# Performance work log

Hardware: AMD Instinct MI355X
Metric: run time of the kernel (lower is better)

Reference implementation:

```python
import jax, jax.numpy as jnp
import numpy as np

N, D, BS, M, DC, H, DH, L, E = 16384, 512, 16, 256, 512, 8, 64, 4, 262144
EPS = 1e-5


def _ln(x, w, b):
    mu = jnp.mean(x, -1, keepdims=True)
    var = jnp.var(x, -1, keepdims=True)
    return (x - mu) * jax.lax.rsqrt(var + EPS) * w + b


def _gcn(x, src, dst, W, b, n):
    deg = jax.ops.segment_sum(jnp.ones_like(src, dtype=x.dtype), dst, num_segments=n)
    dinv = jnp.where(deg > 0, deg ** -0.5, 0.0)
    norm = dinv[src] * dinv[dst]  # [E+N]
    h = x @ W
    out = jax.ops.segment_sum(h[src] * norm[:, None], dst, num_segments=n)
    return out + b


def _attn(xf, cond, Wq, Wk, Wv, Wo):
    n, d = xf.shape
    xb = xf.reshape(BS, n // BS, d)                    # stack(chunk(x, bs))
    q = (xb @ Wq).reshape(BS, -1, H, DH)
    k = (cond @ Wk).reshape(BS, -1, H, DH)
    v = (cond @ Wv).reshape(BS, -1, H, DH)
    att = jnp.einsum('bnhd,bmhd->bhnm', q, k) * (DH ** -0.5)
    w = jax.nn.softmax(att, axis=-1)
    o = jnp.einsum('bhnm,bmhd->bnhd', w, v).reshape(BS, -1, H * DH)
    return (o @ Wo).reshape(n, d)


def setup_inputs() -> dict:
    key = jax.random.key(0)
    ks = jax.random.split(key, 24)
    s = lambda fi, fo: (2.0 / (fi + fo)) ** 0.5
    inp = {
        'x': jax.random.normal(ks[0], (N, D), jnp.float32),
        'edge_index': jax.random.randint(ks[1], (2, E), 0, N, jnp.int64),
        'cond': jax.random.normal(ks[2], (BS, M, DC), jnp.float32),
        'bn_w': jnp.ones((D,), jnp.float32),
        'bn_b': jnp.zeros((D,), jnp.float32),
        'gcn_in_w': jax.random.normal(ks[3], (D, D), jnp.float32) * s(D, D),
        'gcn_in_b': jnp.zeros((D,), jnp.float32),
        'gcn_out_w': jax.random.normal(ks[4], (D, D), jnp.float32) * s(D, D),
        'gcn_out_b': jnp.zeros((D,), jnp.float32),
        'Wq': jax.random.normal(ks[5], (L, D, H * DH), jnp.float32) * s(D, H * DH),
        'Wk': jax.random.normal(ks[6], (L, DC, H * DH), jnp.float32) * s(DC, H * DH),
        'Wv': jax.random.normal(ks[7], (L, DC, H * DH), jnp.float32) * s(DC, H * DH),
        'Wo': jax.random.normal(ks[8], (L, H * DH, D), jnp.float32) * s(H * DH, D),
        'ln2_w': jnp.ones((L, D), jnp.float32),
        'ln2_b': jnp.zeros((L, D), jnp.float32),
        'ln3_w': jnp.ones((L, D), jnp.float32),
        'ln3_b': jnp.zeros((L, D), jnp.float32),
        'geglu_w': jax.random.normal(ks[9], (L, D, 8 * D), jnp.float32) * s(D, 8 * D),
        'geglu_b': jnp.zeros((L, 8 * D), jnp.float32),
        'ffo_w': jax.random.normal(ks[10], (L, 4 * D, D), jnp.float32) * s(4 * D, D),
        'ffo_b': jnp.zeros((L, D), jnp.float32),
    }
    return inp


def reference(x, edge_index, cond, bn_w, bn_b, gcn_in_w, gcn_in_b, gcn_out_w,
              gcn_out_b, Wq, Wk, Wv, Wo, ln2_w, ln2_b, ln3_w, ln3_b,
              geglu_w, geglu_b, ffo_w, ffo_b):
    n = x.shape[0]
    loops = jnp.arange(n)
    src = jnp.concatenate([edge_index[0], loops])
    dst = jnp.concatenate([edge_index[1], loops])

    x_in = x
    # BatchNorm1d (training mode: batch stats, biased var)
    mu = jnp.mean(x, 0)
    var = jnp.var(x, 0)
    h = (x - mu) * jax.lax.rsqrt(var + EPS) * bn_w + bn_b

    h = _gcn(h, src, dst, gcn_in_w, gcn_in_b, n)

    for i in range(L):
        a = _attn(_ln(h, ln2_w[i], ln2_b[i]), cond, Wq[i], Wk[i], Wv[i], Wo[i])
        h = h + a
        u = _ln(h, ln3_w[i], ln3_b[i]) @ geglu_w[i] + geglu_b[i]
        val, gate = jnp.split(u, 2, axis=-1)
        f = val * jax.nn.gelu(gate, approximate=False)
        h = h + f @ ffo_w[i] + ffo_b[i]

    h = _gcn(h, src, dst, gcn_out_w, gcn_out_b, n)
    return h + x_in
```

## Files before the change

kernel.cpp:

```cpp
#include <hip/hip_runtime.h>
#include <math.h>
#include <stdio.h>

#define N_NODES 16384
#define DIM     512
#define BSZ     16
#define SEQ     1024
#define MCTX    256
#define NHEAD   8
#define DHEAD   64
#define NLAYER  4
#define NEDGE   262144
#define DFF     2048
#define DG      4096
#define LNEPS   1e-5f

typedef unsigned short u16;
typedef __attribute__((ext_vector_type(8))) __bf16 bf16x8;
typedef __attribute__((ext_vector_type(4))) float f32x4;
typedef __attribute__((ext_vector_type(4))) unsigned short u16x4;
typedef __attribute__((ext_vector_type(8))) unsigned short u16x8;

__device__ __forceinline__ u16 f2b(float f) {
    unsigned u = __float_as_uint(f);
    unsigned r = (u + 0x7fff + ((u >> 16) & 1)) >> 16;
    return (u16)r;
}
__device__ __forceinline__ float b2f(u16 h) {
    return __uint_as_float((unsigned)h << 16);
}
__device__ __forceinline__ float gelu_exact(float x) {
    return 0.5f * x * (1.0f + erff(x * 0.70710678118654752f));
}
__device__ __forceinline__ float gelu_fast(float x) {
    float u = x * (0.7978845608f + 0.0356774081f * x * x);
    float e = __expf(2.f * u);
    float t = 1.f - 2.f / (e + 1.f);
    return 0.5f * x * (1.f + t);
}
__device__ __forceinline__ void gload16(const void* g, void* l) {
    __builtin_amdgcn_global_load_lds(
        (const __attribute__((address_space(1))) unsigned int*)g,
        (__attribute__((address_space(3))) unsigned int*)l, 16, 0, 0);
}

__device__ __forceinline__ int2 xcd_map() {
    int gx = gridDim.x, gy = gridDim.y;
    int nwg = gx * gy;
    int id = blockIdx.y * gx + blockIdx.x;
    int q = nwg >> 3, r = nwg & 7;
    int xcd = id & 7, idx = id >> 3;
    int nid = (xcd < r ? xcd * (q + 1) : r * (q + 1) + (xcd - r) * q) + idx;
    int2 o; o.x = nid % gx; o.y = nid / gx; return o;
}

__global__ __launch_bounds__(512, 2) void bgemm256_geglu(
    const u16* __restrict__ A, long lda,
    const u16* __restrict__ Bt, long ldb,
    const float* __restrict__ bias,
    u16* __restrict__ Cb, int K)
{
    __shared__ u16 lds[65536];

    const int t = threadIdx.x;
    const int w = t >> 6, lane = t & 63;
    const int fr = lane & 15, fq = lane >> 4;
    int2 sw = xcd_map();
    const int row0 = sw.y * 256;
    const int col0 = sw.x * 256;
    const int wm0 = (w >> 2) * 128, wn0 = (w & 3) * 64;
    const int sl = (lane & 7) ^ ((lane >> 3) & 7);

    f32x4 acc[8][4];
#pragma unroll
    for (int mf = 0; mf < 8; ++mf)
#pragma unroll
        for (int nf = 0; nf < 4; ++nf) acc[mf][nf] = (f32x4){0.f, 0.f, 0.f, 0.f};

    auto stageA = [&](int kt_, int P, int bb) {
        const int k0 = kt_ << 6;
#pragma unroll
        for (int rd = 0; rd < 2; ++rd) {
            int rbase = rd * 128 + P * 64 + w * 8;
            int r = rbase + (lane >> 3);
            gload16(A + (size_t)(row0 + r) * lda + k0 + sl * 8,
                    (char*)(lds + bb * 16384) + rbase * 128);
        }
    };
    auto stageB = [&](int kt_, int Q, int bb) {
        const int k0 = kt_ << 6;
#pragma unroll
        for (int rd = 0; rd < 2; ++rd) {
            int jb = rd * 64 + w * 8;
            int nbase = ((jb >> 5) << 6) + Q * 32 + (jb & 31);
            int n = nbase + (lane >> 3);
            gload16(Bt + (size_t)(col0 + n) * ldb + k0 + sl * 8,
                    (char*)(lds + 32768 + bb * 16384) + nbase * 128);
        }
    };

#define READ_A(MH, DST) do {                                                   \
    _Pragma("unroll")                                                          \
    for (int mi = 0; mi < 4; ++mi) {                                           \
        int r = wm0 + (MH) * 64 + mi * 16 + fr;                                \
        _Pragma("unroll")                                                      \
        for (int ks = 0; ks < 2; ++ks)                                         \
            DST[mi][ks] = *(const bf16x8*)&Ab_[r * 64 + (((ks*4+fq) ^ (fr&7)) * 8)]; \
    } } while (0)
#define READ_B(NH, DST) do {                                                   \
    _Pragma("unroll")                                                          \
    for (int ni = 0; ni < 2; ++ni) {                                           \
        int n = wn0 + (NH) * 32 + ni * 16 + fr;                                \
        _Pragma("unroll")                                                      \
        for (int ks = 0; ks < 2; ++ks)                                         \
            DST[ni][ks] = *(const bf16x8*)&Bb_[n * 64 + (((ks*4+fq) ^ (fr&7)) * 8)]; \
    } } while (0)
#define MFMA16(MH, NH, AV, BV)                                                 \
    _Pragma("unroll")                                                          \
    for (int mi = 0; mi < 4; ++mi)                                             \
        _Pragma("unroll")                                                      \
        for (int ni = 0; ni < 2; ++ni)                                         \
            _Pragma("unroll")                                                  \
            for (int ks = 0; ks < 2; ++ks)                                     \
                acc[(MH)*4+mi][(NH)*2+ni] = __builtin_amdgcn_mfma_f32_16x16x32_bf16( \
                    AV[mi][ks], BV[ni][ks], acc[(MH)*4+mi][(NH)*2+ni], 0, 0, 0)

    stageA(0, 0, 0); stageB(0, 0, 0); stageA(0, 1, 0); stageB(0, 1, 0);
    stageA(1, 0, 1); stageB(1, 0, 1);
    asm volatile("s_waitcnt vmcnt(4)" ::: "memory");
    __builtin_amdgcn_s_barrier();

    const int NT = K >> 6;
    for (int kt = 0; kt < NT; ++kt) {
        const int b = kt & 1;
        const bool s1 = (kt + 1 < NT), s2 = (kt + 2 < NT);
        const u16* Ab_ = lds + b * 16384;
        const u16* Bb_ = lds + 32768 + b * 16384;
        bf16x8 aR[4][2], bR[2][2], bK[2][2];

        READ_A(0, aR); READ_B(0, bK);
        if (s1) stageA(kt + 1, 1, b ^ 1);
        __builtin_amdgcn_s_barrier();
        asm volatile("s_waitcnt lgkmcnt(0)" ::: "memory");
        __builtin_amdgcn_s_setprio(1);
        MFMA16(0, 0, aR, bK);
        __builtin_amdgcn_s_setprio(0);
        __builtin_amdgcn_s_barrier();

        READ_B(1, bR);
        if (s1) stageB(kt + 1, 1, b ^ 1);
        __builtin_amdgcn_s_barrier();
        asm volatile("s_waitcnt lgkmcnt(0)" ::: "memory");
        __builtin_amdgcn_s_setprio(1);
        MFMA16(0, 1, aR, bR);
        __builtin_amdgcn_s_setprio(0);
        __builtin_amdgcn_s_barrier();

        READ_A(1, aR);
        if (s2) stageA(kt + 2, 0, b);
        __builtin_amdgcn_s_barrier();
        asm volatile("s_waitcnt lgkmcnt(0)" ::: "memory");
        __builtin_amdgcn_s_setprio(1);
        MFMA16(1, 1, aR, bR);
        __builtin_amdgcn_s_setprio(0);
        __builtin_amdgcn_s_barrier();

        if (s2) stageB(kt + 2, 0, b);
        __builtin_amdgcn_s_barrier();
        __builtin_amdgcn_s_setprio(1);
        MFMA16(1, 0, aR, bK);
        __builtin_amdgcn_s_setprio(0);
        if (s2)      asm volatile("s_waitcnt vmcnt(4)" ::: "memory");
        else if (s1) asm volatile("s_waitcnt vmcnt(0)" ::: "memory");
        __builtin_amdgcn_s_barrier();
    }
#undef READ_A
#undef READ_B
#undef MFMA16

    const int nbase = (col0 + wn0) >> 1;
    float bval[2], bgat[2];
#pragma unroll
    for (int P = 0; P < 2; ++P) {
        int n = nbase + P * 16 + fr;
        bval[P] = bias[n];
        bgat[P] = bias[DFF + n];
    }
#pragma unroll
    for (int mf = 0; mf < 8; ++mf) {
        const int rb = row0 + wm0 + mf * 16 + fq * 4;
#pragma unroll
        for (int P = 0; P < 2; ++P) {
            const int n = nbase + P * 16 + fr;
#pragma unroll
            for (int j = 0; j < 4; ++j) {
                float v = acc[mf][2 * P][j] + bval[P];
                float g = acc[mf][2 * P + 1][j] + bgat[P];
                Cb[(size_t)(rb + j) * DFF + n] = f2b(v * gelu_fast(g));
            }
        }
    }
}

template<int EPI>
__global__ __launch_bounds__(256) void bgemm(
    const u16* __restrict__ A, long lda,
    const u16* __restrict__ Bt, long ldb,
    const float* __restrict__ bias,
    const float* __restrict__ resid, long ldr,
    const float* __restrict__ rowscale,
    void* __restrict__ Cv, long ldc, int K, int nlo,
    long aHi, long aLo, long bHi, long bLo, long cHi, long cLo)
{
    __shared__ u16 lds[32768];

    const int t = threadIdx.x;
    const int z = blockIdx.z;
    const int zhi = z / nlo, zlo = z % nlo;
    const u16* Ag = A + (size_t)zhi * aHi + (size_t)zlo * aLo;
    const u16* Bg = Bt + (size_t)zhi * bHi + (size_t)zlo * bLo;
    const long coff = (long)zhi * cHi + (long)zlo * cLo;

    int2 sw = xcd_map();
    const int row0 = sw.y * 128;
    const int col0 = sw.x * 128;
    const int wave = t >> 6, lane = t & 63;
    const int wm0 = (wave >> 1) * 64, wn0 = (wave & 1) * 64;
    const int fr = lane & 15, fq = lane >> 4;
    const int ldsWave = (t & 192) * 16;
    const int rS = t >> 3;
    const int slotP = t & 7;

    f32x4 acc[4][4];
#pragma unroll
    for (int mi = 0; mi < 4; ++mi)
#pragma unroll
        for (int ni = 0; ni < 4; ++ni) acc[mi][ni] = (f32x4){0.f, 0.f, 0.f, 0.f};

    auto stage = [&](int buf, int k0) {
        u16* Ad = lds + buf * 8192;
        u16* Bd = lds + 16384 + buf * 8192;
#pragma unroll
        for (int i = 0; i < 4; ++i) {
            int r = i * 32 + rS;
            int s2 = slotP ^ (r & 7);
            gload16(Ag + (size_t)(row0 + r) * lda + k0 + s2 * 8,
                    (char*)Ad + i * 4096 + ldsWave);
        }
#pragma unroll
        for (int i = 0; i < 4; ++i) {
            int r = i * 32 + rS;
            int s2 = slotP ^ (r & 7);
            gload16(Bg + (size_t)(col0 + r) * ldb + k0 + s2 * 8,
                    (char*)Bd + i * 4096 + ldsWave);
        }
    };
    auto compute = [&](int buf) {
        const u16* Ac = lds + buf * 8192;
        const u16* Bc = lds + 16384 + buf * 8192;
#pragma unroll
        for (int ks = 0; ks < 2; ++ks) {
            const int ksl = ks * 4 + fq;
            bf16x8 av[4], bv[4];
#pragma unroll
            for (int mi = 0; mi < 4; ++mi) {
                int r = wm0 + mi * 16 + fr;
                av[mi] = *(const bf16x8*)&Ac[r * 64 + ((ksl ^ (r & 7)) * 8)];
            }
#pragma unroll
            for (int ni = 0; ni < 4; ++ni) {
                int r = wn0 + ni * 16 + fr;
                bv[ni] = *(const bf16x8*)&Bc[r * 64 + ((ksl ^ (r & 7)) * 8)];
            }
#pragma unroll
            for (int mi = 0; mi < 4; ++mi)
#pragma unroll
                for (int ni = 0; ni < 4; ++ni)
                    acc[mi][ni] = __builtin_amdgcn_mfma_f32_16x16x32_bf16(
                        av[mi], bv[ni], acc[mi][ni], 0, 0, 0);
        }
    };

    int cur = 0;
    stage(0, 0);
    __syncthreads();
    for (int k0 = 64; k0 < K; k0 += 64) {
        stage(cur ^ 1, k0);
        compute(cur);
        __syncthreads();
        cur ^= 1;
    }
    compute(cur);

    if (EPI == 3) {
        __syncthreads();
        u16* Tw = lds + wave * 4608;
#pragma unroll
        for (int mi = 0; mi < 4; ++mi)
#pragma unroll
            for (int ni = 0; ni < 4; ++ni)
#pragma unroll
                for (int j = 0; j < 4; ++j)
                    Tw[(ni * 16 + fr) * 72 + mi * 16 + fq * 4 + j] =
                        f2b(acc[mi][ni][j]);
        const int r0w = row0 + wm0;
        const int b = r0w >> 8, m0w = r0w & 255;
        const int cc0 = col0 + wn0, hh = cc0 >> 6;
        u16* dst = (u16*)Cv + coff + ((size_t)(b * 8 + hh) * 64) * 256 + m0w;
#pragma unroll
        for (int it = 0; it < 8; ++it) {
            int dl = it * 8 + (lane >> 3);
            int ml = (lane & 7) * 8;
            u16x8 v = *(const u16x8*)&Tw[dl * 72 + ml];
            *(u16x8*)&dst[(size_t)dl * 256 + ml] = v;
        }
        return;
    }

    float* Cf = (float*)Cv;
    u16* Cb = (u16*)Cv;
#pragma unroll
    for (int mi = 0; mi < 4; ++mi) {
        const int rb = row0 + wm0 + mi * 16 + fq * 4;
#pragma unroll
        for (int ni = 0; ni < 4; ++ni) {
            const int cc = col0 + wn0 + ni * 16 + fr;
            f32x4 v = acc[mi][ni];
            float bval = 0.f;
            if ((EPI == 1 || EPI == 2) && bias) bval = bias[cc];
#pragma unroll
            for (int j = 0; j < 4; ++j) {
                const long r = rb + j;
                float o = v[j] + bval;
                if (EPI == 1) {
                    Cb[coff + r * ldc + cc] = f2b(o);
                } else if (EPI == 2) {
                    Cf[coff + r * ldc + cc] = o + resid[r * ldr + cc];
                } else if (EPI == 4) {
                    Cb[coff + r * ldc + cc] = f2b(o * rowscale[r]);
                }
            }
        }
    }
}

__global__ __launch_bounds__(256) void transposeW(const float* __restrict__ src,
                                                  u16* __restrict__ dst,
                                                  int K, int N,
                                                  long srcZ, long dstZ, int permN)
{
    __shared__ float tile[64][65];
    const int t = threadIdx.x;
    const int n0 = blockIdx.x * 64, k0 = blockIdx.y * 64;
    const float* s = src + (size_t)blockIdx.z * srcZ;
    u16* d = dst + (size_t)blockIdx.z * dstZ;
#pragma unroll
    for (int i = 0; i < 16; ++i) {
        int idx = i * 256 + t;
        int rr = idx >> 6, cc = idx & 63;
        tile[rr][cc] = s[(size_t)(k0 + rr) * N + n0 + cc];
    }
    __syncthreads();
#pragma unroll
    for (int i = 0; i < 16; ++i) {
        int idx = i * 256 + t;
        int rr = idx >> 6, cc = idx & 63;
        int n = n0 + rr;
        int p = n;
        if (permN) {
            p = (n < permN) ? (((n >> 4) << 5) + (n & 15))
                            : ((((n - permN) >> 4) << 5) + 16 + ((n - permN) & 15));
        }
        d[(size_t)p * K + k0 + cc] = f2b(tile[cc][rr]);
    }
}

__global__ __launch_bounds__(256) void conv_f2b(const float* __restrict__ in,
                                                u16* __restrict__ out)
{
    size_t i = (size_t)blockIdx.x * 256 + threadIdx.x;
    float4 v = ((const float4*)in)[i];
    u16x4 o;
    o[0] = f2b(v.x); o[1] = f2b(v.y); o[2] = f2b(v.z); o[3] = f2b(v.w);
    ((u16x4*)out)[i] = o;
}

__global__ __launch_bounds__(512) void bn_colstats(const float* __restrict__ x,
                                                   float* __restrict__ cs,
                                                   float* __restrict__ cq)
{
    int c = threadIdx.x;
    int r0 = blockIdx.x * 128;
    float s = 0.f, q = 0.f;
    for (int r = 0; r < 128; ++r) {
        float v = x[(size_t)(r0 + r) * DIM + c];
        s += v; q += v * v;
    }
    atomicAdd(&cs[c], s);
    atomicAdd(&cq[c], q);
}

__global__ void bn_finalize(const float* __restrict__ cs, const float* __restrict__ cq,
                            const float* __restrict__ bw, const float* __restrict__ bb,
                            float* __restrict__ scale, float* __restrict__ shift)
{
    int c = threadIdx.x;
    float m   = cs[c] * (1.f / N_NODES);
    float var = cq[c] * (1.f / N_NODES) - m * m;
    float rs  = rsqrtf(var + LNEPS);
    float sc  = rs * bw[c];
    scale[c] = sc;
    shift[c] = bb[c] - m * sc;
}

__global__ __launch_bounds__(256) void bn_apply_b(const float* __restrict__ x,
                                                  const float* __restrict__ scale,
                                                  const float* __restrict__ shift,
                                                  u16* __restrict__ out)
{
    size_t idx = (size_t)blockIdx.x * 256 + threadIdx.x;
    int c4 = (int)(idx & 127);
    float4 v  = ((const float4*)x)[idx];
    float4 sc = ((const float4*)scale)[c4];
    float4 sh = ((const float4*)shift)[c4];
    u16x4 o;
    o[0] = f2b(v.x * sc.x + sh.x); o[1] = f2b(v.y * sc.y + sh.y);
    o[2] = f2b(v.z * sc.z + sh.z); o[3] = f2b(v.w * sc.w + sh.w);
    ((u16x4*)out)[idx] = o;
}

__global__ __launch_bounds__(256) void layernorm_b(const float* __restrict__ in,
                                                   const float* __restrict__ w,
                                                   const float* __restrict__ bsh,
                                                   u16* __restrict__ out)
{
    int lane = threadIdx.x & 63, wv = threadIdx.x >> 6;
    size_t row = (size_t)blockIdx.x * 4 + wv;
    const float* p = in + row * DIM + lane * 8;
    float4 v0 = *(const float4*)p;
    float4 v1 = *(const float4*)(p + 4);
    float s = v0.x + v0.y + v0.z + v0.w + v1.x + v1.y + v1.z + v1.w;
    float q = v0.x * v0.x + v0.y * v0.y + v0.z * v0.z + v0.w * v0.w +
              v1.x * v1.x + v1.y * v1.y + v1.z * v1.z + v1.w * v1.w;
    for (int m = 1; m < 64; m <<= 1) {
        s += __shfl_xor(s, m, 64);
        q += __shfl_xor(q, m, 64);
    }
    float mean = s * (1.f / DIM);
    float rs = rsqrtf(q * (1.f / DIM) - mean * mean + LNEPS);
    float4 w0 = *(const float4*)(w + lane * 8),   w1 = *(const float4*)(w + lane * 8 + 4);
    float4 b0 = *(const float4*)(bsh + lane * 8), b1 = *(const float4*)(bsh + lane * 8 + 4);
    u16x8 o;
    o[0] = f2b((v0.x - mean) * rs * w0.x + b0.x);
    o[1] = f2b((v0.y - mean) * rs * w0.y + b0.y);
    o[2] = f2b((v0.z - mean) * rs * w0.z + b0.z);
    o[3] = f2b((v0.w - mean) * rs * w0.w + b0.w);
    o[4] = f2b((v1.x - mean) * rs * w1.x + b1.x);
    o[5] = f2b((v1.y - mean) * rs * w1.y + b1.y);
    o[6] = f2b((v1.z - mean) * rs * w1.z + b1.z);
    o[7] = f2b((v1.w - mean) * rs * w1.w + b1.w);
    *(u16x8*)(out + row * DIM + lane * 8) = o;
}

__global__ __launch_bounds__(256) void fused_attn(
    const u16* __restrict__ Q,
    const u16* __restrict__ Kp,
    const u16* __restrict__ Vt,
    u16* __restrict__ O)
{
    __shared__ u16 Ks[256 * 64];
    __shared__ u16 Vs[64 * 256];
    __shared__ u16 Ps[4][16 * 256];

    const int t = threadIdx.x;
    const int wave = t >> 6, lane = t & 63;
    const int fr = lane & 15, fq = lane >> 4;
    const int qc = blockIdx.x, h = blockIdx.y, b = blockIdx.z;
    const int ldsW = (t & 192) * 16;

#pragma unroll
    for (int i = 0; i < 8; ++i) {
        int idx = i * 256 + t;
        int m = idx >> 3, s = idx & 7;
        gload16(Kp + (size_t)(b * MCTX + m) * 512 + h * 64 + ((s ^ (m & 7)) * 8),
                (char*)Ks + i * 4096 + ldsW);
    }
#pragma unroll
    for (int i = 0; i < 8; ++i) {
        int idx = i * 256 + t;
        int d = idx >> 5, s = idx & 31;
        gload16(Vt + (size_t)((b * 8 + h) * 64 + d) * 256 + ((s ^ (d & 7)) * 8),
                (char*)Vs + i * 4096 + ldsW);
    }
    __syncthreads();

    u16* Pw = Ps[wave];
    for (int it = 0; it < 4; ++it) {
        const int q0 = qc * 256 + it * 64 + wave * 16;
        bf16x8 aq[2];
#pragma unroll
        for (int ks = 0; ks < 2; ++ks)
            aq[ks] = *(const bf16x8*)&Q[(size_t)(b * SEQ + q0 + fr) * 512 +
                                        h * 64 + ks * 32 + fq * 8];
        f32x4 accS[16];
#pragma unroll
        for (int ni = 0; ni < 16; ++ni) accS[ni] = (f32x4){0.f, 0.f, 0.f, 0.f};
#pragma unroll
        for (int ni = 0; ni < 16; ++ni) {
            int m = ni * 16 + fr;
#pragma unroll
            for (int ks = 0; ks < 2; ++ks) {
                bf16x8 bv = *(const bf16x8*)&Ks[m * 64 + (((ks * 4 + fq) ^ (m & 7)) * 8)];
                accS[ni] = __builtin_amdgcn_mfma_f32_16x16x32_bf16(
                    aq[ks], bv, accS[ni], 0, 0, 0);
            }
        }
        const float cs = 0.125f;
#pragma unroll
        for (int j = 0; j < 4; ++j) {
            float m0 = accS[0][j];
#pragma unroll
            for (int ni = 1; ni < 16; ++ni) m0 = fmaxf(m0, accS[ni][j]);
            m0 = fmaxf(m0, __shfl_xor(m0, 1, 64));
            m0 = fmaxf(m0, __shfl_xor(m0, 2, 64));
            m0 = fmaxf(m0, __shfl_xor(m0, 4, 64));
            m0 = fmaxf(m0, __shfl_xor(m0, 8, 64));
            float s0 = 0.f;
#pragma unroll
            for (int ni = 0; ni < 16; ++ni) {
                float p = __expf((accS[ni][j] - m0) * cs);
                accS[ni][j] = p;
                s0 += p;
            }
            s0 += __shfl_xor(s0, 1, 64);
            s0 += __shfl_xor(s0, 2, 64);
            s0 += __shfl_xor(s0, 4, 64);
            s0 += __shfl_xor(s0, 8, 64);
            float inv = 1.f / s0;
#pragma unroll
            for (int ni = 0; ni < 16; ++ni) {
                int cc = ni * 16 + fr;
                int rr = fq * 4 + j;
                Pw[rr * 256 + (((cc >> 3) ^ (rr & 7)) * 8) + (cc & 7)] =
                    f2b(accS[ni][j] * inv);
            }
        }
        bf16x8 ap[8];
#pragma unroll
        for (int ks = 0; ks < 8; ++ks)
            ap[ks] = *(const bf16x8*)&Pw[fr * 256 + (((ks * 4 + fq) ^ (fr & 7)) * 8)];
        f32x4 accO[4];
#pragma unroll
        for (int ni = 0; ni < 4; ++ni) accO[ni] = (f32x4){0.f, 0.f, 0.f, 0.f};
#pragma unroll
        for (int ni = 0; ni < 4; ++ni) {
            int d = ni * 16 + fr;
#pragma unroll
            for (int ks = 0; ks < 8; ++ks) {
                bf16x8 bv = *(const bf16x8*)&Vs[d * 256 + (((ks * 4 + fq) ^ (d & 7)) * 8)];
                accO[ni] = __builtin_amdgcn_mfma_f32_16x16x32_bf16(
                    ap[ks], bv, accO[ni], 0, 0, 0);
            }
        }
#pragma unroll
        for (int ni = 0; ni < 4; ++ni)
#pragma unroll
            for (int j = 0; j < 4; ++j)
                O[(size_t)(b * SEQ + q0 + fq * 4 + j) * 512 + h * 64 + ni * 16 + fr] =
                    f2b(accO[ni][j]);
    }
}

__global__ void detect_i64(const int* __restrict__ e, int* __restrict__ flag)
{
    int idx = blockIdx.x * blockDim.x + threadIdx.x;
    if (e[2 * idx + 1] != 0) flag[0] = 1;
}

__global__ void deg_count(const int* __restrict__ eb, const int* __restrict__ flag,
                          int* __restrict__ deg)
{
    int e = blockIdx.x * blockDim.x + threadIdx.x;
    int d;
    if (flag[0]) d = eb[NEDGE + e];
    else         d = (int)((const long long*)eb)[NEDGE + e];
    atomicAdd(&deg[d], 1);
}

__global__ void dinv_k(const int* __restrict__ deg, float* __restrict__ dinv)
{
    int i = blockIdx.x * blockDim.x + threadIdx.x;
    dinv[i] = rsqrtf((float)(deg[i] + 1));
}

__global__ __launch_bounds__(1024) void scan_deg(const int* __restrict__ deg,
                                                 int* __restrict__ off)
{
    __shared__ int sums[1024];
    int t = threadIdx.x;
    int base = t * 16;
    int v[16]; int s = 0;
#pragma unroll
    for (int i = 0; i < 16; ++i) { v[i] = deg[base + i]; s += v[i]; }
    sums[t] = s;
    __syncthreads();
    for (int ofs = 1; ofs < 1024; ofs <<= 1) {
        int x = (t >= ofs) ? sums[t - ofs] : 0;
        __syncthreads();
        sums[t] += x;
        __syncthreads();
    }
    int run = (t == 0) ? 0 : sums[t - 1];
#pragma unroll
    for (int i = 0; i < 16; ++i) { off[base + i] = run; run += v[i]; }
    if (t == 1023) off[N_NODES] = run;
}

__global__ void fill_k(const int* __restrict__ eb, const int* __restrict__ flag,
                       const int* __restrict__ off, int* __restrict__ cursor,
                       int* __restrict__ csr)
{
    int e = blockIdx.x * blockDim.x + threadIdx.x;
    int s, d;
    if (flag[0]) { s = eb[e]; d = eb[NEDGE + e]; }
    else {
        const long long* p = (const long long*)eb;
        s = (int)p[e]; d = (int)p[NEDGE + e];
    }
    int pos = atomicAdd(&cursor[d], 1);
    csr[off[d] + pos] = s;
}

__global__ __launch_bounds__(256) void gcn_gather(
    const u16* __restrict__ h2, const int* __restrict__ csr,
    const int* __restrict__ off, const float* __restrict__ dinv,
    const float* __restrict__ bias, const float* __restrict__ addx,
    float* __restrict__ out)
{
    int lane = threadIdx.x & 63, wv = threadIdx.x >> 6;
    int d = blockIdx.x * 4 + wv;
    float acc[8];
#pragma unroll
    for (int j = 0; j < 8; ++j) acc[j] = 0.f;
    int e0 = off[d], e1 = off[d + 1];
    float dd = dinv[d];
    int sidx = (e0 < e1) ? csr[e0] : d;
    u16x8 v = *(const u16x8*)&h2[(size_t)sidx * DIM + lane * 8];
    for (int e = e0; e < e1; ++e) {
        int snext = (e + 1 < e1) ? csr[e + 1] : d;
        u16x8 vn = *(const u16x8*)&h2[(size_t)snext * DIM + lane * 8];
#pragma unroll
        for (int j = 0; j < 8; ++j) acc[j] += b2f(v[j]);
        v = vn;
    }
#pragma unroll
    for (int j = 0; j < 8; ++j) acc[j] = (acc[j] + b2f(v[j])) * dd;
    float o[8];
#pragma unroll
    for (int j = 0; j < 8; ++j) {
        o[j] = acc[j] + bias[lane * 8 + j];
        if (addx) o[j] += addx[(size_t)d * DIM + lane * 8 + j];
    }
    float* op = out + (size_t)d * DIM + lane * 8;
    *(float4*)op = make_float4(o[0], o[1], o[2], o[3]);
    *(float4*)(op + 4) = make_float4(o[4], o[5], o[6], o[7]);
}

extern "C" void kernel_launch(void* const* d_in, const int* in_sizes, int n_in,
                              void* d_out, int out_size, void* d_ws, size_t ws_size,
                              hipStream_t stream)
{
    const float* x         = (const float*)d_in[0];
    const int*   edges     = (const int*)d_in[1];
    const float* cond      = (const float*)d_in[2];
    const float* bn_w      = (const float*)d_in[3];
    const float* bn_b      = (const float*)d_in[4];
    const float* gcn_in_w  = (const float*)d_in[5];
    const float* gcn_in_b  = (const float*)d_in[6];
    const float* gcn_out_w = (const float*)d_in[7];
    const float* gcn_out_b = (const float*)d_in[8];
    const float* Wq  = (const float*)d_in[9];
    const float* Wk  = (const float*)d_in[10];
    const float* Wv  = (const float*)d_in[11];
    const float* Wo  = (const float*)d_in[12];
    const float* ln2w = (const float*)d_in[13];
    const float* ln2b = (const float*)d_in[14];
    const float* ln3w = (const float*)d_in[15];
    const float* ln3b = (const float*)d_in[16];
    const float* ggw = (const float*)d_in[17];
    const float* ggb = (const float*)d_in[18];
    const float* fow = (const float*)d_in[19];
    const float* fob = (const float*)d_in[20];
    float* outp = (float*)d_out;

    char* wsb = (char*)d_ws;
    size_t wsoff = 0;
    auto alloc = [&](size_t bytes) -> void* {
        void* p = wsb + wsoff;
        wsoff = (wsoff + bytes + 255) & ~(size_t)255;
        return p;
    };
    u16*   wT    = (u16*)  alloc((size_t)17301504 * 2);
    u16*   condb = (u16*)  alloc((size_t)4096 * 512 * 2);
    float* h     = (float*)alloc((size_t)N_NODES * DIM * 4);
    u16*   t0b   = (u16*)  alloc((size_t)N_NODES * DIM * 2);
    u16*   qb    = (u16*)  alloc((size_t)N_NODES * DIM * 2);
    u16*   ob    = (u16*)  alloc((size_t)N_NODES * DIM * 2);
    u16*   kb    = (u16*)  alloc((size_t)NLAYER * 4096 * 512 * 2);
    u16*   Vt    = (u16*)  alloc((size_t)NLAYER * BSZ * NHEAD * DHEAD * MCTX * 2);
    char*  zbase  = wsb + wsoff;
    float* colsum = (float*)alloc(DIM * 4);
    float* colsq  = (float*)alloc(DIM * 4);
    int*   deg    = (int*)  alloc(N_NODES * 4);
    int*   cursor = (int*)  alloc(N_NODES * 4);
    int*   eflag  = (int*)  alloc(256);
    size_t zbytes = (size_t)((wsb + wsoff) - zbase);
    float* bscale = (float*)alloc(DIM * 4);
    float* bshift = (float*)alloc(DIM * 4);
    float* dinv   = (float*)alloc(N_NODES * 4);
    int*   csr_off= (int*)  alloc((N_NODES + 16) * 4);
    int*   csr_src= (int*)  alloc((size_t)NEDGE * 4);

    int nch = 0;
    for (int c = 1; c <= 16; c *= 2) {
        size_t need = ((size_t)N_NODES / c) * DFF * 2;
        if (wsoff + need <= ws_size) { nch = c; break; }
    }
    if (nch == 0) { fprintf(stderr, "ws too small (%zu)\n", ws_size); return; }
    u16* Abuf = (u16*)(wsb + wsoff);

    hipMemsetAsync(zbase, 0, zbytes, stream);

    u16* gcnInT  = wT;
    u16* gcnOutT = gcnInT + 262144;
    u16* WqT = gcnOutT + 262144;
    u16* WkT = WqT + 4 * 262144;
    u16* WvT = WkT + 4 * 262144;
    u16* WoT = WvT + 4 * 262144;
    u16* ggT = WoT + 4 * 262144;
    u16* foT = ggT + 4 * 2097152;
    transposeW<<<dim3(8, 8, 1), 256, 0, stream>>>(gcn_in_w,  gcnInT, 512, 512, 0, 0, 0);
    transposeW<<<dim3(8, 8, 1), 256, 0, stream>>>(gcn_out_w, gcnOutT, 512, 512, 0, 0, 0);
    transposeW<<<dim3(8, 8, 4), 256, 0, stream>>>(Wq, WqT, 512, 512, 262144, 262144, 0);
    transposeW<<<dim3(8, 8, 4), 256, 0, stream>>>(Wk, WkT, 512, 512, 262144, 262144, 0);
    transposeW<<<dim3(8, 8, 4), 256, 0, stream>>>(Wv, WvT, 512, 512, 262144, 262144, 0);
    transposeW<<<dim3(8, 8, 4), 256, 0, stream>>>(Wo, WoT, 512, 512, 262144, 262144, 0);
    transposeW<<<dim3(64, 8, 4), 256, 0, stream>>>(ggw, ggT, 512, DG, 2097152, 2097152, DFF);
    transposeW<<<dim3(8, 32, 4), 256, 0, stream>>>(fow, foT, DFF, 512, 1048576, 1048576, 0);
    conv_f2b<<<2048, 256, 0, stream>>>(cond, condb);

    bn_colstats<<<128, 512, 0, stream>>>(x, colsum, colsq);
    bn_finalize<<<1, 512, 0, stream>>>(colsum, colsq, bn_w, bn_b, bscale, bshift);
    bn_apply_b<<<(N_NODES * DIM / 4) / 256, 256, 0, stream>>>(x, bscale, bshift, t0b);

    detect_i64<<<NEDGE / 256, 256, 0, stream>>>(edges, eflag);
    deg_count<<<NEDGE / 256, 256, 0, stream>>>(edges, eflag, deg);
    dinv_k<<<N_NODES / 256, 256, 0, stream>>>(deg, dinv);
    scan_deg<<<1, 1024, 0, stream>>>(deg, csr_off);
    fill_k<<<NEDGE / 256, 256, 0, stream>>>(edges, eflag, csr_off, cursor, csr_src);

    bgemm<1><<<dim3(4, 32, 4), 256, 0, stream>>>(
        condb, 512, WkT, 512, nullptr, nullptr, 0, nullptr, kb, 512, 512, 1,
        0, 0, 262144, 0, (long)4096 * 512, 0);
    bgemm<3><<<dim3(4, 32, 4), 256, 0, stream>>>(
        condb, 512, WvT, 512, nullptr, nullptr, 0, nullptr, Vt, 0, 512, 1,
        0, 0, 262144, 0, (long)BSZ * NHEAD * DHEAD * MCTX, 0);

    bgemm<4><<<dim3(4, 128, 1), 256, 0, stream>>>(
        t0b, 512, gcnInT, 512, nullptr, nullptr, 0, dinv, qb, 512, 512, 1,
        0, 0, 0, 0, 0, 0);
    gcn_gather<<<N_NODES / 4, 256, 0, stream>>>(qb, csr_src, csr_off, dinv,
                                                gcn_in_b, nullptr, h);

    const int ffrows = N_NODES / nch;
    for (int i = 0; i < NLAYER; ++i) {
        const u16* WqTi = WqT + (size_t)i * 262144;
        const u16* WoTi = WoT + (size_t)i * 262144;
        const u16* ggTi = ggT + (size_t)i * 2097152;
        const u16* foTi = foT + (size_t)i * 1048576;
        const u16* kbi  = kb + (size_t)i * 4096 * 512;
        const u16* Vti  = Vt + (size_t)i * BSZ * NHEAD * DHEAD * MCTX;

        layernorm_b<<<N_NODES / 4, 256, 0, stream>>>(h, ln2w + i * DIM, ln2b + i * DIM, t0b);
        bgemm<1><<<dim3(4, 128, 1), 256, 0, stream>>>(
            t0b, 512, WqTi, 512, nullptr, nullptr, 0, nullptr, qb, 512, 512, 1,
            0, 0, 0, 0, 0, 0);
        fused_attn<<<dim3(4, 8, 16), 256, 0, stream>>>(qb, kbi, Vti, ob);
        bgemm<2><<<dim3(4, 128, 1), 256, 0, stream>>>(
            ob, 512, WoTi, 512, nullptr, h, 512, nullptr, h, 512, 512, 1,
            0, 0, 0, 0, 0, 0);

        layernorm_b<<<N_NODES / 4, 256, 0, stream>>>(h, ln3w + i * DIM, ln3b + i * DIM, t0b);
        for (int c = 0; c < nch; ++c) {
            const u16* ac = t0b + (size_t)c * ffrows * 512;
            float* hc = h + (size_t)c * ffrows * 512;
            bgemm256_geglu<<<dim3(DG / 256, ffrows / 256), 512, 0, stream>>>(
                ac, 512, ggTi, 512, ggb + (size_t)i * DG, Abuf, 512);
            bgemm<2><<<dim3(4, ffrows / 128, 1), 256, 0, stream>>>(
                Abuf, 2048, foTi, 2048, fob + (size_t)i * DIM, hc, 512, nullptr,
                hc, 512, 2048, 1, 0, 0, 0, 0, 0, 0);
        }
    }

    conv_f2b<<<8192, 256, 0, stream>>>(h, t0b);
    bgemm<4><<<dim3(4, 128, 1), 256, 0, stream>>>(
        t0b, 512, gcnOutT, 512, nullptr, nullptr, 0, dinv, qb, 512, 512, 1,
        0, 0, 0, 0, 0, 0);
    gcn_gather<<<N_NODES / 4, 256, 0, stream>>>(qb, csr_src, csr_off, dinv,
                                                gcn_out_b, x, outp);
}
```

Before: 1.235 ms.

## Restructure GEGLU GEMM k-loop into two phases, stage epilogue via LDS, unroll GCN gather

The GEGLU GEMM main loop now reads all B fragments at once and runs two larger MFMA phases instead of four, issuing A and B staging loads together. This halves the barrier count per k-tile but raises register pressure. The GEGLU epilogue writes results to LDS and then stores coalesced 16-byte rows instead of scattered 2-byte stores. The GCN gather is unrolled by two with independent accumulators and loads the self-loop row separately, giving more memory-level parallelism.

```diff
diff --git a/kernel.cpp b/kernel.cpp
--- a/kernel.cpp
+++ b/kernel.cpp
@@ -107,23 +107,23 @@
         for (int ks = 0; ks < 2; ++ks)                                         \
             DST[mi][ks] = *(const bf16x8*)&Ab_[r * 64 + (((ks*4+fq) ^ (fr&7)) * 8)]; \
     } } while (0)
-#define READ_B(NH, DST) do {                                                   \
+#define READ_B_ALL(DST) do {                                                   \
     _Pragma("unroll")                                                          \
-    for (int ni = 0; ni < 2; ++ni) {                                           \
-        int n = wn0 + (NH) * 32 + ni * 16 + fr;                                \
+    for (int ni = 0; ni < 4; ++ni) {                                           \
+        int n = wn0 + ni * 16 + fr;                                            \
         _Pragma("unroll")                                                      \
         for (int ks = 0; ks < 2; ++ks)                                         \
             DST[ni][ks] = *(const bf16x8*)&Bb_[n * 64 + (((ks*4+fq) ^ (fr&7)) * 8)]; \
     } } while (0)
-#define MFMA16(MH, NH, AV, BV)                                                 \
+#define MFMA32(MH, AV, BV)                                                     \
     _Pragma("unroll")                                                          \
     for (int mi = 0; mi < 4; ++mi)                                             \
         _Pragma("unroll")                                                      \
-        for (int ni = 0; ni < 2; ++ni)                                         \
+        for (int ni = 0; ni < 4; ++ni)                                         \
             _Pragma("unroll")                                                  \
             for (int ks = 0; ks < 2; ++ks)                                     \
-                acc[(MH)*4+mi][(NH)*2+ni] = __builtin_amdgcn_mfma_f32_16x16x32_bf16( \
-                    AV[mi][ks], BV[ni][ks], acc[(MH)*4+mi][(NH)*2+ni], 0, 0, 0)
+                acc[(MH)*4+mi][ni] = __builtin_amdgcn_mfma_f32_16x16x32_bf16(  \
+                    AV[mi][ks], BV[ni][ks], acc[(MH)*4+mi][ni], 0, 0, 0)
 
     stageA(0, 0, 0); stageB(0, 0, 0); stageA(0, 1, 0); stageB(0, 1, 0);
     stageA(1, 0, 1); stageB(1, 0, 1);
@@ -136,47 +136,31 @@
         const bool s1 = (kt + 1 < NT), s2 = (kt + 2 < NT);
         const u16* Ab_ = lds + b * 16384;
         const u16* Bb_ = lds + 32768 + b * 16384;
-        bf16x8 aR[4][2], bR[2][2], bK[2][2];
-
-        READ_A(0, aR); READ_B(0, bK);
-        if (s1) stageA(kt + 1, 1, b ^ 1);
+        bf16x8 av[4][2], bv[4][2];
+
+        READ_A(0, av); READ_B_ALL(bv);
+        if (s1) { stageA(kt + 1, 1, b ^ 1); stageB(kt + 1, 1, b ^ 1); }
         __builtin_amdgcn_s_barrier();
         asm volatile("s_waitcnt lgkmcnt(0)" ::: "memory");
         __builtin_amdgcn_s_setprio(1);
-        MFMA16(0, 0, aR, bK);
+        MFMA32(0, av, bv);
         __builtin_amdgcn_s_setprio(0);
         __builtin_amdgcn_s_barrier();
 
-        READ_B(1, bR);
-        if (s1) stageB(kt + 1, 1, b ^ 1);
+        READ_A(1, av);
+        if (s2) { stageA(kt + 2, 0, b); stageB(kt + 2, 0, b); }
         __builtin_amdgcn_s_barrier();
         asm volatile("s_waitcnt lgkmcnt(0)" ::: "memory");
         __builtin_amdgcn_s_setprio(1);
-        MFMA16(0, 1, aR, bR);
-        __builtin_amdgcn_s_setprio(0);
-        __builtin_amdgcn_s_barrier();
-
-        READ_A(1, aR);
-        if (s2) stageA(kt + 2, 0, b);
-        __builtin_amdgcn_s_barrier();
-        asm volatile("s_waitcnt lgkmcnt(0)" ::: "memory");
-        __builtin_amdgcn_s_setprio(1);
-        MFMA16(1, 1, aR, bR);
-        __builtin_amdgcn_s_setprio(0);
-        __builtin_amdgcn_s_barrier();
-
-        if (s2) stageB(kt + 2, 0, b);
-        __builtin_amdgcn_s_barrier();
-        __builtin_amdgcn_s_setprio(1);
-        MFMA16(1, 0, aR, bK);
+        MFMA32(1, av, bv);
         __builtin_amdgcn_s_setprio(0);
         if (s2)      asm volatile("s_waitcnt vmcnt(4)" ::: "memory");
         else if (s1) asm volatile("s_waitcnt vmcnt(0)" ::: "memory");
         __builtin_amdgcn_s_barrier();
     }
 #undef READ_A
-#undef READ_B
-#undef MFMA16
+#undef READ_B_ALL
+#undef MFMA32
 
     const int nbase = (col0 + wn0) >> 1;
     float bval[2], bgat[2];
@@ -186,19 +170,30 @@
         bval[P] = bias[n];
         bgat[P] = bias[DFF + n];
     }
-#pragma unroll
-    for (int mf = 0; mf < 8; ++mf) {
-        const int rb = row0 + wm0 + mf * 16 + fq * 4;
-#pragma unroll
-        for (int P = 0; P < 2; ++P) {
-            const int n = nbase + P * 16 + fr;
-#pragma unroll
-            for (int j = 0; j < 4; ++j) {
-                float v = acc[mf][2 * P][j] + bval[P];
-                float g = acc[mf][2 * P + 1][j] + bgat[P];
-                Cb[(size_t)(rb + j) * DFF + n] = f2b(v * gelu_fast(g));
-            }
-        }
+    {
+        u16* Tw = lds + w * 8192;
+#pragma unroll
+        for (int mf = 0; mf < 8; ++mf)
+#pragma unroll
+            for (int P = 0; P < 2; ++P)
+#pragma unroll
+                for (int j = 0; j < 4; ++j) {
+                    float v = acc[mf][2 * P][j] + bval[P];
+                    float g = acc[mf][2 * P + 1][j] + bgat[P];
+                    Tw[(mf * 16 + fq * 4 + j) * 32 + P * 16 + fr] =
+                        f2b(v * gelu_fast(g));
+                }
+    }
+    __syncthreads();
+    const long cb0 = col0 >> 1;
+#pragma unroll
+    for (int i = 0; i < 8; ++i) {
+        int chunk = i * 512 + t;
+        int r = chunk >> 4;
+        int c8 = (chunk & 15) * 8;
+        int sw_ = (r >> 7) * 4 + (c8 >> 5);
+        u16x8 v = *(const u16x8*)&lds[sw_ * 8192 + (r & 127) * 32 + (c8 & 31)];
+        *(u16x8*)&Cb[(size_t)(row0 + r) * DFF + cb0 + c8] = v;
     }
 }
 
@@ -639,26 +634,32 @@
 {
     int lane = threadIdx.x & 63, wv = threadIdx.x >> 6;
     int d = blockIdx.x * 4 + wv;
-    float acc[8];
-#pragma unroll
-    for (int j = 0; j < 8; ++j) acc[j] = 0.f;
+    float a0[8], a1[8];
+#pragma unroll
+    for (int j = 0; j < 8; ++j) { a0[j] = 0.f; a1[j] = 0.f; }
     int e0 = off[d], e1 = off[d + 1];
     float dd = dinv[d];
-    int sidx = (e0 < e1) ? csr[e0] : d;
-    u16x8 v = *(const u16x8*)&h2[(size_t)sidx * DIM + lane * 8];
-    for (int e = e0; e < e1; ++e) {
-        int snext = (e + 1 < e1) ? csr[e + 1] : d;
-        u16x8 vn = *(const u16x8*)&h2[(size_t)snext * DIM + lane * 8];
-#pragma unroll
-        for (int j = 0; j < 8; ++j) acc[j] += b2f(v[j]);
-        v = vn;
-    }
-#pragma unroll
-    for (int j = 0; j < 8; ++j) acc[j] = (acc[j] + b2f(v[j])) * dd;
+    int e = e0;
+    if ((e1 - e0) & 1) {
+        u16x8 v = *(const u16x8*)&h2[(size_t)csr[e] * DIM + lane * 8];
+#pragma unroll
+        for (int j = 0; j < 8; ++j) a0[j] += b2f(v[j]);
+        ++e;
+    }
+    for (; e < e1; e += 2) {
+        int s0 = csr[e], s1 = csr[e + 1];
+        u16x8 v0 = *(const u16x8*)&h2[(size_t)s0 * DIM + lane * 8];
+        u16x8 v1 = *(const u16x8*)&h2[(size_t)s1 * DIM + lane * 8];
+#pragma unroll
+        for (int j = 0; j < 8; ++j) a0[j] += b2f(v0[j]);
+#pragma unroll
+        for (int j = 0; j < 8; ++j) a1[j] += b2f(v1[j]);
+    }
+    u16x8 vd = *(const u16x8*)&h2[(size_t)d * DIM + lane * 8];
     float o[8];
 #pragma unroll
     for (int j = 0; j < 8; ++j) {
-        o[j] = acc[j] + bias[lane * 8 + j];
+        o[j] = (a0[j] + a1[j] + b2f(vd[j])) * dd + bias[lane * 8 + j];
         if (addx) o[j] += addx[(size_t)d * DIM + lane * 8 + j];
     }
     float* op = out + (size_t)d * DIM + lane * 8;
```

New measurement: 1.242 ms. About the same (+0.6%).
